# Performance work log

Hardware: AMD Instinct MI355X
Metric: run time of the kernel (lower is better)

Reference implementation:

```python
import jax, jax.numpy as jnp
import numpy as np

H_DIM = 64
GRID = 8
NBR = 2.0
BN_EPS = 1e-5
N_SEQ = 64
N_PED = 64
BOTTLENECK = 1024


def setup_inputs() -> dict:
    key = jax.random.key(0)
    k0, k1, k2, k3 = jax.random.split(key, 4)
    batch = N_SEQ * N_PED
    h_states = jax.random.normal(k0, (1, batch, H_DIM), jnp.float32)
    # positions spread over a 4x4 area so some neighbors fall inside the 2.0 neighborhood
    end_pos = jax.random.uniform(k1, (batch, 2), jnp.float32) * 4.0
    rel_pos = jax.random.normal(k2, (batch, 2), jnp.float32)
    starts = jnp.arange(N_SEQ, dtype=jnp.int32) * N_PED
    seq_start_end = jnp.stack([starts, starts + N_PED], axis=1)
    in_dim = GRID * GRID * H_DIM  # 4096
    W = jax.random.normal(k3, (in_dim, BOTTLENECK), jnp.float32) / np.sqrt(in_dim)
    b = jnp.zeros((BOTTLENECK,), jnp.float32)
    gamma = jnp.ones((BOTTLENECK,), jnp.float32)
    beta = jnp.zeros((BOTTLENECK,), jnp.float32)
    return {"h_states": h_states, "seq_start_end": seq_start_end, "end_pos": end_pos,
            "rel_pos": rel_pos, "W": W, "b": b, "gamma": gamma, "beta": beta}


def _pool_scene(hidden, pos):
    # hidden: (n, h), pos: (n, 2). Pair (i, j): ped j binned into ped i's grid.
    n, h = hidden.shape
    g2 = GRID * GRID
    half = NBR / 2.0
    tl_x = pos[:, 0] - half
    tl_y = pos[:, 1] + half
    br_x = pos[:, 0] + half
    br_y = pos[:, 1] - half
    px = pos[None, :, 0]  # (1, n) -> broadcast over i
    py = pos[None, :, 1]
    cell_x = jnp.floor((px - tl_x[:, None]) / NBR * GRID)
    cell_y = jnp.floor((tl_y[:, None] - py) / NBR * GRID)
    grid = (cell_x + cell_y * GRID).astype(jnp.int32) + 1  # slot 0 = trash bin
    oob = ((px >= br_x[:, None]) | (px <= tl_x[:, None]) |
           (py >= tl_y[:, None]) | (py <= br_y[:, None]) |
           jnp.eye(n, dtype=bool))  # self-interaction excluded
    grid = grid + (jnp.arange(n, dtype=jnp.int32) * g2)[:, None]
    grid = jnp.where(oob, 0, grid)  # (n, n)
    src = jnp.broadcast_to(hidden[None], (n, n, h)).reshape(-1, h)
    buf = jnp.zeros((n * g2 + 1, h), hidden.dtype).at[grid.reshape(-1)].add(src)
    return buf[1:].reshape(n, g2 * h)


def reference(h_states, seq_start_end, end_pos, rel_pos, W, b, gamma, beta):
    batch = end_pos.shape[0]
    n_seq = seq_start_end.shape[0]
    n_ped = batch // n_seq  # equal-length scenes by construction
    hid = h_states.reshape(-1, H_DIM).reshape(n_seq, n_ped, H_DIM)
    pos = end_pos.reshape(n_seq, n_ped, 2)
    pool_h = jax.vmap(_pool_scene)(hid, pos).reshape(batch, -1)  # (batch, 4096)
    x = pool_h @ W + b
    # BatchNorm1d in training mode (batch statistics, biased variance)
    mean = jnp.mean(x, axis=0)
    var = jnp.var(x, axis=0)
    x = (x - mean) * jax.lax.rsqrt(var + BN_EPS) * gamma + beta
    return jax.nn.relu(x)
```

## Files before the change

kernel.cpp:

```cpp
#include <hip/hip_runtime.h>
#include <hip/hip_bf16.h>


#define NPED  64
#define BATCH 4096
#define HDIM  64
#define G2    64
#define KDIM  4096
#define NOUT  1024

typedef __attribute__((ext_vector_type(8))) short short8;
typedef __attribute__((ext_vector_type(4))) float f32x4;

__device__ __forceinline__ unsigned short f2bf(float f) {
    __hip_bfloat16 h = __float2bfloat16(f);
    return *reinterpret_cast<unsigned short*>(&h);
}

__device__ __forceinline__ void lds_load16(const void* g, void* l) {
    __builtin_amdgcn_global_load_lds(
        (const __attribute__((address_space(1))) void*)g,
        (__attribute__((address_space(3))) void*)l, 16, 0, 0);
}

__global__ __launch_bounds__(256) void pool_kernel(const float* __restrict__ h,
                                                   const float* __restrict__ pos,
                                                   unsigned short* __restrict__ A2) {
    __shared__ float acc[4][G2 * HDIM];
    __shared__ float pl[NPED * 2];
    int t = threadIdx.x;
    int w = t >> 6, lane = t & 63;
    int p0 = blockIdx.x * 4;
    int sbase = p0 & ~(NPED - 1);
    if (t < 128) pl[t] = pos[sbase * 2 + t];
    #pragma unroll
    for (int c = 0; c < G2; ++c) acc[w][c * HDIM + lane] = 0.f;
    __syncthreads();

    int i = p0 + w;
    int il = i & (NPED - 1);
    float cx0 = pl[2 * il], cy0 = pl[2 * il + 1];
    float tlx = cx0 - 1.f, tly = cy0 + 1.f, brx = cx0 + 1.f, bry = cy0 - 1.f;
    for (int jb = 0; jb < NPED; jb += 8) {
        float hv[8];
        #pragma unroll
        for (int u = 0; u < 8; ++u)
            hv[u] = h[(size_t)(sbase + jb + u) * HDIM + lane];
        #pragma unroll
        for (int u = 0; u < 8; ++u) {
            int j = jb + u;
            float px = pl[2 * j], py = pl[2 * j + 1];
            if (j != il && !(px >= brx || px <= tlx || py >= tly || py <= bry)) {
                int cellx = (int)floorf((px - tlx) * 4.f);
                int celly = (int)floorf((tly - py) * 4.f);
                int cell = cellx + celly * 8;
                if ((unsigned)cell < 64u)
                    atomicAdd(&acc[w][cell * HDIM + lane], hv[u]);
            }
        }
    }
    __syncthreads();

    int mtile = p0 >> 4, r0 = p0 & 15;
    unsigned int* out = (unsigned int*)A2 + (size_t)mtile * 32768 + r0 * 4;
    #pragma unroll
    for (int p = 0; p < 32; ++p) {
        int lin = p * 256 + t;
        int fragidx = lin >> 4;
        int rr = (lin >> 2) & 3, q = lin & 3;
        int k = fragidx * 8 + q * 2;
        unsigned int v = (unsigned int)f2bf(acc[rr][k]) |
                         ((unsigned int)f2bf(acc[rr][k + 1]) << 16);
        out[fragidx * 64 + rr * 4 + q] = v;
    }
}

__global__ __launch_bounds__(256) void wt_kernel(const float* __restrict__ W,
                                                 unsigned short* __restrict__ Wt,
                                                 float* __restrict__ stats) {
    __shared__ unsigned short tile[64][66];
    int k0 = blockIdx.x * 64;
    int n0 = blockIdx.y * 64;
    int t = threadIdx.x;
    if (blockIdx.x == 0 && blockIdx.y < 8) stats[blockIdx.y * 256 + t] = 0.f;
    #pragma unroll
    for (int p = 0; p < 4; ++p) {
        int lin = p * 256 + t;
        int c4 = lin & 15, kl = lin >> 4;
        float4 v = ((const float4*)(W + (size_t)(k0 + kl) * NOUT + n0))[c4];
        tile[c4 * 4 + 0][kl] = f2bf(v.x);
        tile[c4 * 4 + 1][kl] = f2bf(v.y);
        tile[c4 * 4 + 2][kl] = f2bf(v.z);
        tile[c4 * 4 + 3][kl] = f2bf(v.w);
    }
    __syncthreads();
    unsigned int* out = (unsigned int*)Wt;
    #pragma unroll
    for (int p = 0; p < 8; ++p) {
        int lin = p * 256 + t;
        int ku = lin & 31, nl = lin >> 5;
        unsigned int v = (unsigned int)tile[nl][2 * ku] |
                         ((unsigned int)tile[nl][2 * ku + 1] << 16);
        out[(size_t)(n0 + nl) * (KDIM / 2) + (k0 >> 1) + ku] = v;
    }
}

__global__ __launch_bounds__(256, 4) void gemm_kernel(const unsigned short* __restrict__ A2,
                                                      const unsigned short* __restrict__ Bt,
                                                      float* __restrict__ C,
                                                      float* __restrict__ P1) {
    __shared__ __align__(16) unsigned short Bs[128 * 64];
    int t = threadIdx.x;
    int w = t >> 6, lane = t & 63;
    int m0 = blockIdx.x * 128, n0 = blockIdx.y * 128;
    int kbase = blockIdx.z * 2048;
    int wm = (w >> 1) * 64, wn = (w & 1) * 64;

    f32x4 acc[4][4];
    #pragma unroll
    for (int i = 0; i < 4; ++i)
        #pragma unroll
        for (int j = 0; j < 4; ++j)
            acc[i][j] = (f32x4){0.f, 0.f, 0.f, 0.f};

    int rbase = w * 32 + (lane >> 3);
    int koff = ((lane & 7) ^ (lane >> 3)) * 8;
    const unsigned short* Bg = Bt + (size_t)(n0 + rbase) * KDIM + kbase + koff;
    unsigned short* BsW = Bs + w * 2048 + lane * 8;

    const unsigned short* Abase = A2 + (size_t)((m0 + wm) >> 4) * 65536 + lane * 8;
    int ktile0 = kbase >> 5;

    for (int kt = 0; kt < 2048; kt += 64) {
        #pragma unroll
        for (int q = 0; q < 4; ++q)
            lds_load16(Bg + (size_t)q * 8 * KDIM + kt, BsW + q * 512);
        short8 af[2][4];
        int ktile = ktile0 + (kt >> 5);
        #pragma unroll
        for (int kk = 0; kk < 2; ++kk)
            #pragma unroll
            for (int i = 0; i < 4; ++i)
                af[kk][i] = *(const short8*)(Abase + ((size_t)i * 128 + ktile + kk) * 512);
        __syncthreads();
        #pragma unroll
        for (int kk = 0; kk < 2; ++kk) {
            short8 bfr[4];
            int chunk = ((kk * 4 + (lane >> 4)) ^ (lane & 7)) * 8;
            #pragma unroll
            for (int jj = 0; jj < 4; ++jj)
                bfr[jj] = *(const short8*)&Bs[(wn + jj * 16 + (lane & 15)) * 64 + chunk];
            #pragma unroll
            for (int i = 0; i < 4; ++i)
                #pragma unroll
                for (int jj = 0; jj < 4; ++jj)
                    acc[i][jj] = __builtin_amdgcn_mfma_f32_16x16x32_bf16(af[kk][i], bfr[jj], acc[i][jj], 0, 0, 0);
        }
        __syncthreads();
    }

    float* dst = blockIdx.z ? P1 : C;
    int col0 = n0 + wn + (lane & 15);
    int row0 = m0 + wm + ((lane >> 4) << 2);
    #pragma unroll
    for (int i = 0; i < 4; ++i)
        #pragma unroll
        for (int j = 0; j < 4; ++j)
            #pragma unroll
            for (int r = 0; r < 4; ++r)
                dst[(size_t)(row0 + i * 16 + r) * NOUT + col0 + j * 16] = acc[i][j][r];
}

__global__ __launch_bounds__(256) void combine_stats(float* __restrict__ C,
                                                     const float* __restrict__ P1,
                                                     float* __restrict__ stats) {
    int t = threadIdx.x;
    int colchunk = blockIdx.x & 3;
    int rowchunk = blockIdx.x >> 2;
    int col = colchunk * 256 + t;
    size_t base = (size_t)rowchunk * 32 * NOUT + col;
    float s = 0.f, s2 = 0.f;
    #pragma unroll 8
    for (int r = 0; r < 32; ++r) {
        size_t ix = base + (size_t)r * NOUT;
        float v = C[ix] + P1[ix];
        C[ix] = v;
        s += v; s2 += v * v;
    }
    atomicAdd(&stats[col], s);
    atomicAdd(&stats[NOUT + col], s2);
}

__global__ __launch_bounds__(256) void norm_kernel(float* __restrict__ C,
                                                   const float* __restrict__ stats,
                                                   const float* __restrict__ gamma,
                                                   const float* __restrict__ beta) {
    int idx = blockIdx.x * 256 + threadIdx.x;
    int col4 = idx & 255;
    float4 x = ((const float4*)C)[idx];
    float4 s = ((const float4*)stats)[col4];
    float4 q = ((const float4*)(stats + NOUT))[col4];
    float4 g = ((const float4*)gamma)[col4];
    float4 b = ((const float4*)beta)[col4];
    const float inv_n = 1.f / 4096.f;
    float m, inv;
    m = s.x * inv_n; inv = rsqrtf(q.x * inv_n - m * m + 1e-5f); x.x = fmaxf((x.x - m) * inv * g.x + b.x, 0.f);
    m = s.y * inv_n; inv = rsqrtf(q.y * inv_n - m * m + 1e-5f); x.y = fmaxf((x.y - m) * inv * g.y + b.y, 0.f);
    m = s.z * inv_n; inv = rsqrtf(q.z * inv_n - m * m + 1e-5f); x.z = fmaxf((x.z - m) * inv * g.z + b.z, 0.f);
    m = s.w * inv_n; inv = rsqrtf(q.w * inv_n - m * m + 1e-5f); x.w = fmaxf((x.w - m) * inv * g.w + b.w, 0.f);
    ((float4*)C)[idx] = x;
}

extern "C" void kernel_launch(void* const* d_in, const int* in_sizes, int n_in,
                              void* d_out, int out_size, void* d_ws, size_t ws_size,
                              hipStream_t stream) {
    const float* h      = (const float*)d_in[0];
    const float* endpos = (const float*)d_in[2];
    const float* W      = (const float*)d_in[4];
    const float* gamma  = (const float*)d_in[6];
    const float* beta   = (const float*)d_in[7];
    float* C = (float*)d_out;

    char* ws = (char*)d_ws;
    unsigned short* A2 = (unsigned short*)ws;
    unsigned short* Wt = (unsigned short*)(ws + (size_t)BATCH * KDIM * 2);
    float* P1    = (float*)(ws + (size_t)BATCH * KDIM * 2 + (size_t)NOUT * KDIM * 2);
    float* stats = (float*)(ws + (size_t)BATCH * KDIM * 2 + (size_t)NOUT * KDIM * 2
                               + (size_t)BATCH * NOUT * 4);

    pool_kernel<<<BATCH / 4, 256, 0, stream>>>(h, endpos, A2);
    wt_kernel<<<dim3(KDIM / 64, NOUT / 64), 256, 0, stream>>>(W, Wt, stats);
    gemm_kernel<<<dim3(BATCH / 128, NOUT / 128, 2), 256, 0, stream>>>(A2, Wt, C, P1);
    combine_stats<<<512, 256, 0, stream>>>(C, P1, stats);
    norm_kernel<<<(BATCH * NOUT / 4) / 256, 256, 0, stream>>>(C, stats, gamma, beta);
}
```

Before: 174.2 us.

## Enlarge GEMM block tile to 256x128 and split K four ways

The GEMM block tile grows from 128x128 to 256x128. Each wave now computes a 64x128 sub-tile with 32 accumulators, so every B fragment read from LDS is reused across more MFMAs. To keep the grid large, the K split goes from 2 to 4, writing into two extra fp32 partial buffers that combine_stats sums. This trades extra global traffic for partials (four 16MB buffers read and written) and lower occupancy (launch bounds 2) for better LDS reuse.

```diff
diff --git a/kernel.cpp b/kernel.cpp
--- a/kernel.cpp
+++ b/kernel.cpp
@@ -105,22 +105,24 @@
     }
 }
 
-__global__ __launch_bounds__(256, 4) void gemm_kernel(const unsigned short* __restrict__ A2,
+__global__ __launch_bounds__(256, 2) void gemm_kernel(const unsigned short* __restrict__ A2,
                                                       const unsigned short* __restrict__ Bt,
                                                       float* __restrict__ C,
-                                                      float* __restrict__ P1) {
+                                                      float* __restrict__ P1,
+                                                      float* __restrict__ P2,
+                                                      float* __restrict__ P3) {
     __shared__ __align__(16) unsigned short Bs[128 * 64];
     int t = threadIdx.x;
     int w = t >> 6, lane = t & 63;
-    int m0 = blockIdx.x * 128, n0 = blockIdx.y * 128;
-    int kbase = blockIdx.z * 2048;
-    int wm = (w >> 1) * 64, wn = (w & 1) * 64;
-
-    f32x4 acc[4][4];
+    int m0 = blockIdx.x * 256, n0 = blockIdx.y * 128;
+    int kbase = blockIdx.z * 1024;
+    int wm = w * 64;
+
+    f32x4 acc[4][8];
     #pragma unroll
     for (int i = 0; i < 4; ++i)
         #pragma unroll
-        for (int j = 0; j < 4; ++j)
+        for (int j = 0; j < 8; ++j)
             acc[i][j] = (f32x4){0.f, 0.f, 0.f, 0.f};
 
     int rbase = w * 32 + (lane >> 3);
@@ -131,7 +133,7 @@
     const unsigned short* Abase = A2 + (size_t)((m0 + wm) >> 4) * 65536 + lane * 8;
     int ktile0 = kbase >> 5;
 
-    for (int kt = 0; kt < 2048; kt += 64) {
+    for (int kt = 0; kt < 1024; kt += 64) {
         #pragma unroll
         for (int q = 0; q < 4; ++q)
             lds_load16(Bg + (size_t)q * 8 * KDIM + kt, BsW + q * 512);
@@ -145,27 +147,25 @@
         __syncthreads();
         #pragma unroll
         for (int kk = 0; kk < 2; ++kk) {
-            short8 bfr[4];
             int chunk = ((kk * 4 + (lane >> 4)) ^ (lane & 7)) * 8;
             #pragma unroll
-            for (int jj = 0; jj < 4; ++jj)
-                bfr[jj] = *(const short8*)&Bs[(wn + jj * 16 + (lane & 15)) * 64 + chunk];
-            #pragma unroll
-            for (int i = 0; i < 4; ++i)
+            for (int j = 0; j < 8; ++j) {
+                short8 b = *(const short8*)&Bs[(j * 16 + (lane & 15)) * 64 + chunk];
                 #pragma unroll
-                for (int jj = 0; jj < 4; ++jj)
-                    acc[i][jj] = __builtin_amdgcn_mfma_f32_16x16x32_bf16(af[kk][i], bfr[jj], acc[i][jj], 0, 0, 0);
+                for (int i = 0; i < 4; ++i)
+                    acc[i][j] = __builtin_amdgcn_mfma_f32_16x16x32_bf16(af[kk][i], b, acc[i][j], 0, 0, 0);
+            }
         }
         __syncthreads();
     }
 
-    float* dst = blockIdx.z ? P1 : C;
-    int col0 = n0 + wn + (lane & 15);
+    float* dst = blockIdx.z == 0 ? C : blockIdx.z == 1 ? P1 : blockIdx.z == 2 ? P2 : P3;
+    int col0 = n0 + (lane & 15);
     int row0 = m0 + wm + ((lane >> 4) << 2);
     #pragma unroll
     for (int i = 0; i < 4; ++i)
         #pragma unroll
-        for (int j = 0; j < 4; ++j)
+        for (int j = 0; j < 8; ++j)
             #pragma unroll
             for (int r = 0; r < 4; ++r)
                 dst[(size_t)(row0 + i * 16 + r) * NOUT + col0 + j * 16] = acc[i][j][r];
@@ -173,6 +173,8 @@
 
 __global__ __launch_bounds__(256) void combine_stats(float* __restrict__ C,
                                                      const float* __restrict__ P1,
+                                                     const float* __restrict__ P2,
+                                                     const float* __restrict__ P3,
                                                      float* __restrict__ stats) {
     int t = threadIdx.x;
     int colchunk = blockIdx.x & 3;
@@ -180,10 +182,10 @@
     int col = colchunk * 256 + t;
     size_t base = (size_t)rowchunk * 32 * NOUT + col;
     float s = 0.f, s2 = 0.f;
-    #pragma unroll 8
+    #pragma unroll 4
     for (int r = 0; r < 32; ++r) {
         size_t ix = base + (size_t)r * NOUT;
-        float v = C[ix] + P1[ix];
+        float v = (C[ix] + P1[ix]) + (P2[ix] + P3[ix]);
         C[ix] = v;
         s += v; s2 += v * v;
     }
@@ -222,15 +224,17 @@
     float* C = (float*)d_out;
 
     char* ws = (char*)d_ws;
-    unsigned short* A2 = (unsigned short*)ws;
-    unsigned short* Wt = (unsigned short*)(ws + (size_t)BATCH * KDIM * 2);
-    float* P1    = (float*)(ws + (size_t)BATCH * KDIM * 2 + (size_t)NOUT * KDIM * 2);
-    float* stats = (float*)(ws + (size_t)BATCH * KDIM * 2 + (size_t)NOUT * KDIM * 2
-                               + (size_t)BATCH * NOUT * 4);
+    size_t off = 0;
+    unsigned short* A2 = (unsigned short*)(ws + off); off += (size_t)BATCH * KDIM * 2;
+    unsigned short* Wt = (unsigned short*)(ws + off); off += (size_t)NOUT * KDIM * 2;
+    float* P1 = (float*)(ws + off); off += (size_t)BATCH * NOUT * 4;
+    float* P2 = (float*)(ws + off); off += (size_t)BATCH * NOUT * 4;
+    float* P3 = (float*)(ws + off); off += (size_t)BATCH * NOUT * 4;
+    float* stats = (float*)(ws + off);
 
     pool_kernel<<<BATCH / 4, 256, 0, stream>>>(h, endpos, A2);
     wt_kernel<<<dim3(KDIM / 64, NOUT / 64), 256, 0, stream>>>(W, Wt, stats);
-    gemm_kernel<<<dim3(BATCH / 128, NOUT / 128, 2), 256, 0, stream>>>(A2, Wt, C, P1);
-    combine_stats<<<512, 256, 0, stream>>>(C, P1, stats);
+    gemm_kernel<<<dim3(BATCH / 256, NOUT / 128, 4), 256, 0, stream>>>(A2, Wt, C, P1, P2, P3);
+    combine_stats<<<512, 256, 0, stream>>>(C, P1, P2, P3, stats);
     norm_kernel<<<(BATCH * NOUT / 4) / 256, 256, 0, stream>>>(C, stats, gamma, beta);
 }
```

Result: no change. 174.6 us (+0.3%).
